# Kernel tuning notes

Hardware: AMD Instinct MI355X
Metric: run time of the kernel (lower is better)

Reference implementation:

```python
import math
import jax, jax.numpy as jnp
import numpy as np

B, T, C = 2, 2048, 1024
H, HKV, HD = 16, 4, 64  # n_head, n_kv_head, head_dim
G = H // HKV            # GQA groups
WS = 1024               # sliding window size
GATE_CH = 32


def setup_inputs() -> dict:
    key = jax.random.key(0)
    ks = jax.random.split(key, 8)
    x = jax.random.normal(ks[0], (B, T, C), dtype=jnp.float32)
    ve = jax.random.normal(ks[1], (B, T, HKV * HD), dtype=jnp.float32)
    # realistic RoPE tables: half head_dim frequencies
    d = HD // 2
    inv_freq = 1.0 / (10000.0 ** (jnp.arange(d, dtype=jnp.float32) / d))
    angles = jnp.arange(T, dtype=jnp.float32)[:, None] * inv_freq[None, :]  # (T, d)
    cos = jnp.cos(angles)[None, :, None, :]  # (1, T, 1, d)
    sin = jnp.sin(angles)[None, :, None, :]
    s = 0.02
    Wq = s * jax.random.normal(ks[2], (C, H * HD), dtype=jnp.float32)
    Wk = s * jax.random.normal(ks[3], (C, HKV * HD), dtype=jnp.float32)
    Wv = s * jax.random.normal(ks[4], (C, HKV * HD), dtype=jnp.float32)
    Wproj = s * jax.random.normal(ks[5], (C, C), dtype=jnp.float32)
    Wg = s * jax.random.normal(ks[6], (GATE_CH, HKV), dtype=jnp.float32)
    return {"x": x, "ve": ve, "cos": cos, "sin": sin,
            "Wq": Wq, "Wk": Wk, "Wv": Wv, "Wproj": Wproj, "Wg": Wg, "ws": WS}


def _rope(u, cos, sin):
    d = u.shape[-1] // 2
    u1, u2 = u[..., :d], u[..., d:]
    return jnp.concatenate([u1 * cos + u2 * sin, -u1 * sin + u2 * cos], axis=-1)


def _rmsnorm(u):
    eps = jnp.finfo(u.dtype).eps
    return u * jax.lax.rsqrt(jnp.mean(u * u, axis=-1, keepdims=True) + eps)


def reference(x, ve, cos, sin, Wq, Wk, Wv, Wproj, Wg, ws):
    b, t, c = x.shape
    q = (x @ Wq).reshape(b, t, H, HD)
    k = (x @ Wk).reshape(b, t, HKV, HD)
    v = (x @ Wv).reshape(b, t, HKV, HD)
    # value-embedding gate: 2*sigmoid over first 32 channels of x
    gate = 2.0 * jax.nn.sigmoid(x[..., :GATE_CH] @ Wg)  # (b, t, HKV)
    v = v + gate[..., None] * ve.reshape(b, t, HKV, HD)
    q = _rmsnorm(_rope(q, cos, sin))
    k = _rmsnorm(_rope(k, cos, sin))
    # GQA: view q as (b, t, HKV, G, HD), contract against shared k/v per kv-head
    qg = q.reshape(b, t, HKV, G, HD)
    scale = 1.0 / math.sqrt(HD)
    scores = jnp.einsum('bqhgd,bkhd->bhgqk', qg, k) * scale  # (b, HKV, G, t, t)
    pos = jnp.arange(t)
    # key j attends iff i - ws + 1 <= j <= i (sliding causal window)
    mask = (pos[None, :] >= pos[:, None] - ws + 1) & (pos[None, :] <= pos[:, None])
    scores = jnp.where(mask[None, None, None], scores, -jnp.inf)
    attn = jax.nn.softmax(scores, axis=-1)
    y = jnp.einsum('bhgqk,bkhd->bqhgd', attn, v).reshape(b, t, H * HD)
    return y @ Wproj
```

## Files before the change

kernel.cpp:

```cpp
#include <hip/hip_runtime.h>
#include <hip/hip_bf16.h>

#define Bq 2
#define Tq 2048
#define Cq 1024
#define Hq 16
#define HKVq 4
#define HDq 64
#define Gq 4
#define WSq 1024
#define GATE_CHq 32

typedef __attribute__((ext_vector_type(8))) short short8;
typedef __attribute__((ext_vector_type(4))) float f32x4;
typedef __attribute__((ext_vector_type(16))) float f32x16;
typedef __attribute__((ext_vector_type(2))) unsigned int u32x2;
typedef unsigned int u32;
typedef unsigned short u16;

#if __has_builtin(__builtin_amdgcn_exp2f)
#define EXP2(x) __builtin_amdgcn_exp2f(x)
#else
#define EXP2(x) exp2f(x)
#endif

__device__ __forceinline__ u16 f2bf(float f) {
  u32 u = __float_as_uint(f);
  u32 r = (u + 0x7FFFu + ((u >> 16) & 1u)) >> 16;
  return (u16)r;
}
__device__ __forceinline__ float bf2f(u16 u) {
  return __uint_as_float(((u32)u) << 16);
}

__device__ __forceinline__ void gl_lds16(const u16* g, u16* l) {
  __builtin_amdgcn_global_load_lds(
      (const u32 __attribute__((address_space(1)))*)g,
      (u32 __attribute__((address_space(3)))*)l, 16, 0, 0);
}

__global__ __launch_bounds__(256) void qkv_gemm_fused(
    const u16* __restrict__ A, const u16* __restrict__ Bt,
    const float* __restrict__ ve, const float* __restrict__ cosp,
    const float* __restrict__ sinp, const float* __restrict__ gatebuf,
    u16* __restrict__ Qb, u16* __restrict__ Kb, u16* __restrict__ Vtb) {
  __shared__ __attribute__((aligned(16))) u16 As[64 * 128];
  __shared__ __attribute__((aligned(16))) u16 Bs[128 * 128];

  const int bx = blockIdx.x;
  const int bm0 = blockIdx.y * 64, bn0 = bx * 128;
  const int tid = threadIdx.x;
  const int w = tid >> 6, lane = tid & 63;
  const int wm = (w >> 1) * 32, wn = (w & 1) * 64;
  const int quad = lane >> 4, l16 = lane & 15;
  const int K = 1024;

  f32x4 acc[2][4];
#pragma unroll
  for (int mt = 0; mt < 2; mt++)
#pragma unroll
    for (int nt = 0; nt < 4; nt++) acc[mt][nt] = (f32x4){0.f, 0.f, 0.f, 0.f};

  int goffA[4], goffB[8];
#pragma unroll
  for (int i = 0; i < 4; i++) {
    int s = i * 256 + tid;
    int m = s >> 4, gp = s & 15;
    goffA[i] = m * K + (gp ^ (m & 7)) * 8;
  }
#pragma unroll
  for (int i = 0; i < 8; i++) {
    int s = i * 256 + tid;
    int m = s >> 4, gp = s & 15;
    goffB[i] = m * K + (gp ^ (m & 7)) * 8;
  }
  const u16* Ab = A + (long)bm0 * K;
  const u16* Bb = Bt + (long)bn0 * K;

  for (int k0 = 0; k0 < K; k0 += 128) {
    __syncthreads();
#pragma unroll
    for (int i = 0; i < 4; i++)
      gl_lds16(Ab + goffA[i] + k0, &As[(i * 256 + w * 64) * 8]);
#pragma unroll
    for (int i = 0; i < 8; i++)
      gl_lds16(Bb + goffB[i] + k0, &Bs[(i * 256 + w * 64) * 8]);
    __syncthreads();

#pragma unroll
    for (int ks = 0; ks < 4; ks++) {
      short8 af[2], bf[4];
#pragma unroll
      for (int mt = 0; mt < 2; mt++) {
        int ml = wm + mt * 16 + l16;
        af[mt] = *(const short8*)&As[ml * 128 + (((ks * 4 + quad) ^ (ml & 7)) * 8)];
      }
#pragma unroll
      for (int nt = 0; nt < 4; nt++) {
        int nl = wn + nt * 16 + l16;
        bf[nt] = *(const short8*)&Bs[nl * 128 + (((ks * 4 + quad) ^ (nl & 7)) * 8)];
      }
#pragma unroll
      for (int mt = 0; mt < 2; mt++)
#pragma unroll
        for (int nt = 0; nt < 4; nt++)
          acc[mt][nt] = __builtin_amdgcn_mfma_f32_16x16x32_bf16(
              af[mt], bf[nt], acc[mt][nt], 0, 0, 0);
    }
  }

  const int b = bm0 >> 11;
  const int tseq0 = (bm0 & 2047) + wm;

  if (bx < 10) {
    u16* Dst;
    if (bx < 8) {
      int hh = bx * 2 + (w & 1);
      int hkv = hh >> 2, g = hh & 3;
      Dst = Qb + ((long)((b * 4 + hkv) * 4 + g) * Tq) * 64;
    } else {
      int kk = (bx - 8) * 2 + (w & 1);
      Dst = Kb + ((long)(b * 4 + kk) * Tq) * 64;
    }
#pragma unroll
    for (int mt = 0; mt < 2; mt++) {
#pragma unroll
      for (int r = 0; r < 4; r++) {
        int t = tseq0 + mt * 16 + quad * 4 + r;
        float c0 = cosp[t * 32 + l16];
        float s0 = sinp[t * 32 + l16];
        float c1 = cosp[t * 32 + 16 + l16];
        float s1 = sinp[t * 32 + 16 + l16];
        float a0 = acc[mt][0][r], a1 = acc[mt][1][r];
        float a2 = acc[mt][2][r], a3 = acc[mt][3][r];
        float rp0 = a0 * c0 + a2 * s0;
        float rp1 = a1 * c1 + a3 * s1;
        float rp2 = a2 * c0 - a0 * s0;
        float rp3 = a3 * c1 - a1 * s1;
        float ss = rp0 * rp0 + rp1 * rp1 + rp2 * rp2 + rp3 * rp3;
        ss += __shfl_xor(ss, 1);
        ss += __shfl_xor(ss, 2);
        ss += __shfl_xor(ss, 4);
        ss += __shfl_xor(ss, 8);
        float sc = rsqrtf(ss * (1.f / 64.f) + 1.1920928955078125e-07f);
        u16* drow = Dst + (long)t * 64;
        drow[l16] = f2bf(rp0 * sc);
        drow[16 + l16] = f2bf(rp1 * sc);
        drow[32 + l16] = f2bf(rp2 * sc);
        drow[48 + l16] = f2bf(rp3 * sc);
      }
    }
  } else {
    int kk = (bx - 10) * 2 + (w & 1);
    u16* Dst = Vtb + ((long)(b * 4 + kk) * 64) * Tq;
#pragma unroll
    for (int mt = 0; mt < 2; mt++) {
      float vals[4][4];
#pragma unroll
      for (int r = 0; r < 4; r++) {
        int t = tseq0 + mt * 16 + quad * 4 + r;
        long bt = (long)b * Tq + t;
        float gv = gatebuf[bt * 4 + kk];
        const float* verow = ve + bt * 256 + kk * 64;
#pragma unroll
        for (int nt = 0; nt < 4; nt++)
          vals[nt][r] = acc[mt][nt][r] + gv * verow[nt * 16 + l16];
      }
      int t0m = tseq0 + mt * 16 + quad * 4;
#pragma unroll
      for (int nt = 0; nt < 4; nt++) {
        int d = nt * 16 + l16;
        union { short4 v; u16 u[4]; } p;
#pragma unroll
        for (int r = 0; r < 4; r++) p.u[r] = f2bf(vals[nt][r]);
        *(short4*)(Dst + (long)d * Tq + t0m) = p.v;
      }
    }
  }
}

__global__ __launch_bounds__(256) void gemm_proj(
    const u16* __restrict__ A, const u16* __restrict__ Bt,
    float* __restrict__ C, int M, int N, int K) {
  __shared__ __attribute__((aligned(16))) u16 As[64 * 128];
  __shared__ __attribute__((aligned(16))) u16 Bs[128 * 128];

  const int bm0 = blockIdx.y * 64, bn0 = blockIdx.x * 128;
  const int tid = threadIdx.x;
  const int w = tid >> 6, lane = tid & 63;
  const int wm = (w >> 1) * 32, wn = (w & 1) * 64;
  const int quad = lane >> 4, l16 = lane & 15;

  f32x4 acc[2][4];
#pragma unroll
  for (int mt = 0; mt < 2; mt++)
#pragma unroll
    for (int nt = 0; nt < 4; nt++) acc[mt][nt] = (f32x4){0.f, 0.f, 0.f, 0.f};

  int goffA[4], goffB[8];
#pragma unroll
  for (int i = 0; i < 4; i++) {
    int s = i * 256 + tid;
    int m = s >> 4, gp = s & 15;
    goffA[i] = m * K + (gp ^ (m & 7)) * 8;
  }
#pragma unroll
  for (int i = 0; i < 8; i++) {
    int s = i * 256 + tid;
    int m = s >> 4, gp = s & 15;
    goffB[i] = m * K + (gp ^ (m & 7)) * 8;
  }
  const u16* Ab = A + (long)bm0 * K;
  const u16* Bb = Bt + (long)bn0 * K;

  for (int k0 = 0; k0 < K; k0 += 128) {
    __syncthreads();
#pragma unroll
    for (int i = 0; i < 4; i++)
      gl_lds16(Ab + goffA[i] + k0, &As[(i * 256 + w * 64) * 8]);
#pragma unroll
    for (int i = 0; i < 8; i++)
      gl_lds16(Bb + goffB[i] + k0, &Bs[(i * 256 + w * 64) * 8]);
    __syncthreads();

#pragma unroll
    for (int ks = 0; ks < 4; ks++) {
      short8 af[2], bf[4];
#pragma unroll
      for (int mt = 0; mt < 2; mt++) {
        int ml = wm + mt * 16 + l16;
        af[mt] = *(const short8*)&As[ml * 128 + (((ks * 4 + quad) ^ (ml & 7)) * 8)];
      }
#pragma unroll
      for (int nt = 0; nt < 4; nt++) {
        int nl = wn + nt * 16 + l16;
        bf[nt] = *(const short8*)&Bs[nl * 128 + (((ks * 4 + quad) ^ (nl & 7)) * 8)];
      }
#pragma unroll
      for (int mt = 0; mt < 2; mt++)
#pragma unroll
        for (int nt = 0; nt < 4; nt++)
          acc[mt][nt] = __builtin_amdgcn_mfma_f32_16x16x32_bf16(
              af[mt], bf[nt], acc[mt][nt], 0, 0, 0);
    }
  }

#pragma unroll
  for (int mt = 0; mt < 2; mt++)
#pragma unroll
    for (int nt = 0; nt < 4; nt++) {
      int row0 = bm0 + wm + mt * 16 + quad * 4;
      int col = bn0 + wn + nt * 16 + l16;
#pragma unroll
      for (int r = 0; r < 4; r++)
        C[(long)(row0 + r) * N + col] = acc[mt][nt][r];
    }
}

__global__ __launch_bounds__(256) void prep(
    const float* __restrict__ x, u16* __restrict__ xb,
    const float* __restrict__ Wq, const float* __restrict__ Wk,
    const float* __restrict__ Wv, const float* __restrict__ Wproj,
    const float* __restrict__ Wg, u16* __restrict__ Dqkv,
    u16* __restrict__ Dproj, float* __restrict__ gatebuf) {
  __shared__ float tile[64][65];
  int bx = blockIdx.x;
  int tid = threadIdx.x;
  if (bx < 2048) {
    int i = (bx * 256 + tid) * 8;
    float4 a = *(const float4*)(x + i);
    float4 b = *(const float4*)(x + i + 4);
    union { short8 v; u16 u[8]; } o;
    o.u[0] = f2bf(a.x); o.u[1] = f2bf(a.y); o.u[2] = f2bf(a.z); o.u[3] = f2bf(a.w);
    o.u[4] = f2bf(b.x); o.u[5] = f2bf(b.y); o.u[6] = f2bf(b.z); o.u[7] = f2bf(b.w);
    *(short8*)(xb + i) = o.v;
    return;
  }
  if (bx >= 2688) {
    int p = (bx - 2688) * 256 + tid;
    int bt = p >> 2, kk = p & 3;
    const float* xr = x + (long)bt * Cq;
    float dot = 0.f;
#pragma unroll
    for (int i = 0; i < GATE_CHq; i++) dot += xr[i] * Wg[i * HKVq + kk];
    gatebuf[p] = 2.f / (1.f + expf(-dot));
    return;
  }
  int wb = bx - 2048;
  int obx = wb >> 4;
  int k0 = (wb & 15) * 64;
  const float* S;
  u16* Dst;
  int N, nb;
  if (obx < 16)      { S = Wq;    N = 1024; nb = obx;      Dst = Dqkv; }
  else if (obx < 20) { S = Wk;    N = 256;  nb = obx - 16; Dst = Dqkv + 1024 * 1024; }
  else if (obx < 24) { S = Wv;    N = 256;  nb = obx - 20; Dst = Dqkv + 1280 * 1024; }
  else               { S = Wproj; N = 1024; nb = obx - 24; Dst = Dproj; }
  int n0 = nb * 64;
#pragma unroll
  for (int i = 0; i < 16; i++) {
    int idx = i * 256 + tid;
    int kl = idx >> 6, nl = idx & 63;
    tile[kl][nl] = S[(long)(k0 + kl) * N + n0 + nl];
  }
  __syncthreads();
#pragma unroll
  for (int i = 0; i < 16; i++) {
    int idx = i * 256 + tid;
    int nl = idx >> 6, kl = idx & 63;
    Dst[(long)(n0 + nl) * 1024 + k0 + kl] = f2bf(tile[kl][nl]);
  }
}

#define CEXP 0.18033688011112042f
#define CEXP8 1.4426950408889634f

template <bool MASK>
__device__ __forceinline__ void attn_tile32(
    int k0, int q0, int l31, int hl, const u16* __restrict__ Ks,
    const u16* __restrict__ Vts, const short8 (&QB)[4], f32x16& O0, f32x16& O1,
    float& lsum) {
  const int qpos = q0 + l31;
#pragma unroll
  for (int c = 0; c < 4; c++) {
    const int key = c * 32 + l31;
    f32x16 S;
#pragma unroll
    for (int i = 0; i < 16; i++) S[i] = 0.f;
    __builtin_amdgcn_s_setprio(1);
#pragma unroll
    for (int s = 0; s < 4; s++) {
      short8 kf = *(const short8*)&Ks[key * 64 + (((s * 2 + hl) ^ (key & 7)) * 8)];
      S = __builtin_amdgcn_mfma_f32_32x32x16_bf16(kf, QB[s], S, 0, 0, 0);
    }
    __builtin_amdgcn_s_setprio(0);
    const int kb = k0 + c * 32 + 4 * hl;
    float p[16];
    float la0 = 0.f, la1 = 0.f;
#pragma unroll
    for (int r = 0; r < 16; r++) {
      float sv = S[r];
      if (MASK) {
        int kpos = kb + (r & 3) + 8 * (r >> 2);
        u32 diff = (u32)(qpos - kpos);
        sv = (diff < (u32)WSq) ? sv : -1e30f;
      }
      float pv = EXP2(__builtin_fmaf(sv, CEXP, -CEXP8));
      if (r & 1) la1 += pv; else la0 += pv;
      p[r] = pv;
    }
    lsum += la0 + la1;
    u32 w[8];
#pragma unroll
    for (int i = 0; i < 8; i++) {
      u32 lo = __float_as_uint(p[2 * i]) + 0x8000u;
      u32 hi = __float_as_uint(p[2 * i + 1]) + 0x8000u;
      w[i] = __builtin_amdgcn_perm(hi, lo, 0x07060302u);
    }
    u32x2 r02 = __builtin_amdgcn_permlane32_swap(w[0], w[2], false, false);
    u32x2 r13 = __builtin_amdgcn_permlane32_swap(w[1], w[3], false, false);
    u32x2 r46 = __builtin_amdgcn_permlane32_swap(w[4], w[6], false, false);
    u32x2 r57 = __builtin_amdgcn_permlane32_swap(w[5], w[7], false, false);
    union { short8 s8; u32 u[4]; } f0, f1;
    f0.u[0] = r02[0]; f0.u[1] = r13[0]; f0.u[2] = r02[1]; f0.u[3] = r13[1];
    f1.u[0] = r46[0]; f1.u[1] = r57[0]; f1.u[2] = r46[1]; f1.u[3] = r57[1];
    const int d0 = l31, d1 = 32 + l31;
    const int sw = (l31 & 7);
    __builtin_amdgcn_s_setprio(1);
#pragma unroll
    for (int kc = 0; kc < 2; kc++) {
      int grp = c * 4 + kc * 2 + hl;
      short8 v0 = *(const short8*)&Vts[d0 * 128 + ((grp ^ sw) * 8)];
      short8 v1 = *(const short8*)&Vts[d1 * 128 + ((grp ^ sw) * 8)];
      const short8 pf = kc ? f1.s8 : f0.s8;
      O0 = __builtin_amdgcn_mfma_f32_32x32x16_bf16(v0, pf, O0, 0, 0, 0);
      O1 = __builtin_amdgcn_mfma_f32_32x32x16_bf16(v1, pf, O1, 0, 0, 0);
    }
    __builtin_amdgcn_s_setprio(0);
  }
}

__global__ __launch_bounds__(256, 2) void attn_mfma(
    const u16* __restrict__ Qb, const u16* __restrict__ Kb,
    const u16* __restrict__ Vtb, u16* __restrict__ Yb) {
  __shared__ __attribute__((aligned(16))) u16 Ks[2][128 * 64];
  __shared__ __attribute__((aligned(16))) u16 Vts[2][64 * 128];

  int bid = blockIdx.x;
  int bh = bid & 7;
  int qt32 = bid >> 3;
  int hkv = bh & 3;
  int b = bh >> 2;
  int q0 = qt32 * 32;
  int tid = threadIdx.x;
  int g = tid >> 6;
  int lane = tid & 63;
  int l31 = lane & 31;
  int hl = lane >> 5;

  short8 QB[4];
  {
    const u16* qb =
        Qb + ((long)((bh * 4 + g) * Tq + q0 + l31)) * 64 + hl * 8;
#pragma unroll
    for (int s = 0; s < 4; s++) QB[s] = *(const short8*)(qb + s * 16);
  }

  f32x16 O0, O1;
#pragma unroll
  for (int i = 0; i < 16; i++) { O0[i] = 0.f; O1[i] = 0.f; }
  float lsum = 0.f;

  int lo = q0 - (WSq - 1);
  int st = (lo < 0 ? 0 : lo) >> 7;
  int et = (q0 + 31) >> 7;

  const u16* Kbase = Kb + ((long)bh * Tq) * 64;
  const u16* Vbase = Vtb + ((long)bh * 64) * Tq;

  int rowoffK[4], rowoffV[4];
#pragma unroll
  for (int i = 0; i < 4; i++) {
    int s = i * 256 + tid;
    int kr = s >> 3, kgp = s & 7;
    rowoffK[i] = kr * 64 + (kgp ^ (kr & 7)) * 8;
    int d = s >> 4, vgp = s & 15;
    rowoffV[i] = d * Tq + (vgp ^ (d & 7)) * 8;
  }

  {
    int k0 = st << 7;
#pragma unroll
    for (int i = 0; i < 4; i++) {
      gl_lds16(Kbase + (long)k0 * 64 + rowoffK[i], &Ks[0][(i * 256 + g * 64) * 8]);
      gl_lds16(Vbase + k0 + rowoffV[i], &Vts[0][(i * 256 + g * 64) * 8]);
    }
  }
  __syncthreads();

  int cur = 0;
  for (int kt = st; kt <= et; kt++) {
    int k0 = kt << 7;
    if (kt < et) {
      int k0n = k0 + 128;
#pragma unroll
      for (int i = 0; i < 4; i++) {
        gl_lds16(Kbase + (long)k0n * 64 + rowoffK[i],
                 &Ks[cur ^ 1][(i * 256 + g * 64) * 8]);
        gl_lds16(Vbase + k0n + rowoffV[i],
                 &Vts[cur ^ 1][(i * 256 + g * 64) * 8]);
      }
    }
    bool needC = (k0 + 127 > q0);
    bool needW = (k0 < q0 - 992);
    if (needC || needW) {
      attn_tile32<true>(k0, q0, l31, hl, Ks[cur], Vts[cur], QB, O0, O1, lsum);
    } else {
      attn_tile32<false>(k0, q0, l31, hl, Ks[cur], Vts[cur], QB, O0, O1, lsum);
    }
    __syncthreads();
    cur ^= 1;
  }

  lsum += __shfl_xor(lsum, 32);
  float invl = 1.f / lsum;

  int h = hkv * 4 + g;
  u16* yrow = Yb + ((long)(b * Tq + q0 + l31)) * 1024 + h * 64;
#pragma unroll
  for (int g4 = 0; g4 < 4; g4++) {
    union { short4 v; u16 u[4]; } pk0, pk1;
#pragma unroll
    for (int i = 0; i < 4; i++) {
      pk0.u[i] = f2bf(O0[g4 * 4 + i] * invl);
      pk1.u[i] = f2bf(O1[g4 * 4 + i] * invl);
    }
    int dA = 8 * g4 + 4 * hl;
    *(short4*)(yrow + dA) = pk0.v;
    *(short4*)(yrow + 32 + dA) = pk1.v;
  }
}

extern "C" void kernel_launch(void* const* d_in, const int* in_sizes, int n_in,
                              void* d_out, int out_size, void* d_ws,
                              size_t ws_size, hipStream_t stream) {
  const float* x     = (const float*)d_in[0];
  const float* ve    = (const float*)d_in[1];
  const float* cosp  = (const float*)d_in[2];
  const float* sinp  = (const float*)d_in[3];
  const float* Wq    = (const float*)d_in[4];
  const float* Wk    = (const float*)d_in[5];
  const float* Wv    = (const float*)d_in[6];
  const float* Wproj = (const float*)d_in[7];
  const float* Wg    = (const float*)d_in[8];

  char* base = (char*)d_ws;
  u16* xb      = (u16*)(base);
  u16* Yb      = xb;
  u16* WqkvT   = (u16*)(base + 8388608);
  u16* WprojT  = (u16*)(base + 11534336);
  u16* Qb      = (u16*)(base + 13631488);
  u16* Kb      = (u16*)(base + 22020096);
  u16* Vtb     = (u16*)(base + 24117248);
  float* gateb = (float*)(base + 26214400);
  float* out = (float*)d_out;

  prep<<<2752, 256, 0, stream>>>(x, xb, Wq, Wk, Wv, Wproj, Wg, WqkvT, WprojT,
                                 gateb);
  qkv_gemm_fused<<<dim3(12, 64), 256, 0, stream>>>(xb, WqkvT, ve, cosp, sinp,
                                                   gateb, Qb, Kb, Vtb);
  attn_mfma<<<512, 256, 0, stream>>>(Qb, Kb, Vtb, Yb);
  gemm_proj<<<dim3(8, 64), 256, 0, stream>>>(Yb, WprojT, out, 4096, 1024, 1024);
}
```

Measured before the change: 163.5 us.

## Fuse all four stages into one cooperative persistent kernel with grid syncs

Replaces the four launches (prep, QKV GEMM, attention, projection) with a single cooperative kernel of 512 blocks that steps through the stages, separated by grid.sync and thread fences. The QKV GEMM stage is retiled to 128x128 blocks so that 384 blocks cover the work, and the other stages reuse the existing tiling on a shared LDS buffer. The aim is to remove launch gaps and per-kernel tails. In exchange the grid-wide barriers add cost, 128 blocks sit idle during the GEMM stage, and occupancy is capped by the 64KB shared buffer. If the cooperative launch fails, it falls back to the original four launches.

```diff
diff --git a/kernel.cpp b/kernel.cpp
--- a/kernel.cpp
+++ b/kernel.cpp
@@ -1,5 +1,8 @@
 #include <hip/hip_runtime.h>
 #include <hip/hip_bf16.h>
+#include <hip/hip_cooperative_groups.h>
+
+namespace cg = cooperative_groups;
 
 #define Bq 2
 #define Tq 2048
@@ -29,14 +32,451 @@
   u32 r = (u + 0x7FFFu + ((u >> 16) & 1u)) >> 16;
   return (u16)r;
 }
-__device__ __forceinline__ float bf2f(u16 u) {
-  return __uint_as_float(((u32)u) << 16);
-}
 
 __device__ __forceinline__ void gl_lds16(const u16* g, u16* l) {
   __builtin_amdgcn_global_load_lds(
       (const u32 __attribute__((address_space(1)))*)g,
       (u32 __attribute__((address_space(3)))*)l, 16, 0, 0);
+}
+
+#define CEXP 0.18033688011112042f
+#define CEXP8 1.4426950408889634f
+
+template <bool MASK>
+__device__ __forceinline__ void attn_tile32(
+    int k0, int q0, int l31, int hl, const u16* __restrict__ Ks,
+    const u16* __restrict__ Vts, const short8 (&QB)[4], f32x16& O0, f32x16& O1,
+    float& lsum) {
+  const int qpos = q0 + l31;
+#pragma unroll
+  for (int c = 0; c < 4; c++) {
+    const int key = c * 32 + l31;
+    f32x16 S;
+#pragma unroll
+    for (int i = 0; i < 16; i++) S[i] = 0.f;
+    __builtin_amdgcn_s_setprio(1);
+#pragma unroll
+    for (int s = 0; s < 4; s++) {
+      short8 kf = *(const short8*)&Ks[key * 64 + (((s * 2 + hl) ^ (key & 7)) * 8)];
+      S = __builtin_amdgcn_mfma_f32_32x32x16_bf16(kf, QB[s], S, 0, 0, 0);
+    }
+    __builtin_amdgcn_s_setprio(0);
+    const int kb = k0 + c * 32 + 4 * hl;
+    float p[16];
+    float la0 = 0.f, la1 = 0.f;
+#pragma unroll
+    for (int r = 0; r < 16; r++) {
+      float sv = S[r];
+      if (MASK) {
+        int kpos = kb + (r & 3) + 8 * (r >> 2);
+        u32 diff = (u32)(qpos - kpos);
+        sv = (diff < (u32)WSq) ? sv : -1e30f;
+      }
+      float pv = EXP2(__builtin_fmaf(sv, CEXP, -CEXP8));
+      if (r & 1) la1 += pv; else la0 += pv;
+      p[r] = pv;
+    }
+    lsum += la0 + la1;
+    u32 w8[8];
+#pragma unroll
+    for (int i = 0; i < 8; i++) {
+      u32 lo = __float_as_uint(p[2 * i]) + 0x8000u;
+      u32 hi = __float_as_uint(p[2 * i + 1]) + 0x8000u;
+      w8[i] = __builtin_amdgcn_perm(hi, lo, 0x07060302u);
+    }
+    u32x2 r02 = __builtin_amdgcn_permlane32_swap(w8[0], w8[2], false, false);
+    u32x2 r13 = __builtin_amdgcn_permlane32_swap(w8[1], w8[3], false, false);
+    u32x2 r46 = __builtin_amdgcn_permlane32_swap(w8[4], w8[6], false, false);
+    u32x2 r57 = __builtin_amdgcn_permlane32_swap(w8[5], w8[7], false, false);
+    union { short8 s8; u32 u[4]; } f0, f1;
+    f0.u[0] = r02[0]; f0.u[1] = r13[0]; f0.u[2] = r02[1]; f0.u[3] = r13[1];
+    f1.u[0] = r46[0]; f1.u[1] = r57[0]; f1.u[2] = r46[1]; f1.u[3] = r57[1];
+    const int d0 = l31, d1 = 32 + l31;
+    const int sw = (l31 & 7);
+    __builtin_amdgcn_s_setprio(1);
+#pragma unroll
+    for (int kc = 0; kc < 2; kc++) {
+      int grp = c * 4 + kc * 2 + hl;
+      short8 v0 = *(const short8*)&Vts[d0 * 128 + ((grp ^ sw) * 8)];
+      short8 v1 = *(const short8*)&Vts[d1 * 128 + ((grp ^ sw) * 8)];
+      const short8 pf = kc ? f1.s8 : f0.s8;
+      O0 = __builtin_amdgcn_mfma_f32_32x32x16_bf16(v0, pf, O0, 0, 0, 0);
+      O1 = __builtin_amdgcn_mfma_f32_32x32x16_bf16(v1, pf, O1, 0, 0, 0);
+    }
+    __builtin_amdgcn_s_setprio(0);
+  }
+}
+
+__global__ __launch_bounds__(256, 2) void mega(
+    const float* __restrict__ x, const float* __restrict__ ve,
+    const float* __restrict__ cosp, const float* __restrict__ sinp,
+    const float* __restrict__ Wq, const float* __restrict__ Wk,
+    const float* __restrict__ Wv, const float* __restrict__ Wproj,
+    const float* __restrict__ Wg, u16* __restrict__ xb,
+    u16* __restrict__ WqkvT, u16* __restrict__ WprojT, u16* __restrict__ Qb,
+    u16* __restrict__ Kb, u16* __restrict__ Vtb, float* __restrict__ gateb,
+    float* __restrict__ out) {
+  __shared__ __attribute__((aligned(16))) u16 smem[32768];
+  cg::grid_group grid = cg::this_grid();
+
+  const int bid = blockIdx.x;
+  const int tid = threadIdx.x;
+  const int w = tid >> 6, lane = tid & 63;
+  const int quad = lane >> 4, l16 = lane & 15;
+
+  for (int vb = bid; vb < 2752; vb += 512) {
+    if (vb < 2048) {
+      int i = (vb * 256 + tid) * 8;
+      float4 a = *(const float4*)(x + i);
+      float4 b4 = *(const float4*)(x + i + 4);
+      union { short8 v; u16 u[8]; } o;
+      o.u[0] = f2bf(a.x); o.u[1] = f2bf(a.y); o.u[2] = f2bf(a.z); o.u[3] = f2bf(a.w);
+      o.u[4] = f2bf(b4.x); o.u[5] = f2bf(b4.y); o.u[6] = f2bf(b4.z); o.u[7] = f2bf(b4.w);
+      *(short8*)(xb + i) = o.v;
+    } else if (vb >= 2688) {
+      int p = (vb - 2688) * 256 + tid;
+      int bt = p >> 2, kk = p & 3;
+      const float* xr = x + (long)bt * Cq;
+      float dot = 0.f;
+#pragma unroll
+      for (int i = 0; i < GATE_CHq; i++) dot += xr[i] * Wg[i * HKVq + kk];
+      gateb[p] = 2.f / (1.f + expf(-dot));
+    } else {
+      float* tile = (float*)smem;
+      int wb = vb - 2048;
+      int obx = wb >> 4;
+      int k0 = (wb & 15) * 64;
+      const float* S;
+      u16* Dst;
+      int N, nb;
+      if (obx < 16)      { S = Wq;    N = 1024; nb = obx;      Dst = WqkvT; }
+      else if (obx < 20) { S = Wk;    N = 256;  nb = obx - 16; Dst = WqkvT + 1024 * 1024; }
+      else if (obx < 24) { S = Wv;    N = 256;  nb = obx - 20; Dst = WqkvT + 1280 * 1024; }
+      else               { S = Wproj; N = 1024; nb = obx - 24; Dst = WprojT; }
+      int n0 = nb * 64;
+#pragma unroll
+      for (int i = 0; i < 16; i++) {
+        int idx = i * 256 + tid;
+        int kl = idx >> 6, nl = idx & 63;
+        tile[kl * 65 + nl] = S[(long)(k0 + kl) * N + n0 + nl];
+      }
+      __syncthreads();
+#pragma unroll
+      for (int i = 0; i < 16; i++) {
+        int idx = i * 256 + tid;
+        int nl = idx >> 6, kl = idx & 63;
+        Dst[(long)(n0 + nl) * 1024 + k0 + kl] = f2bf(tile[kl * 65 + nl]);
+      }
+      __syncthreads();
+    }
+  }
+  __threadfence();
+  grid.sync();
+  __threadfence();
+
+  if (bid < 384) {
+    const int bx = bid % 12;
+    const int bm0 = (bid / 12) * 128, bn0 = bx * 128;
+    const int wm = (w >> 1) * 64, wn = (w & 1) * 64;
+    const int K = 1024;
+    u16* sA = smem;
+    u16* sB = smem + 16384;
+
+    f32x4 acc[4][4];
+#pragma unroll
+    for (int mt = 0; mt < 4; mt++)
+#pragma unroll
+      for (int nt = 0; nt < 4; nt++) acc[mt][nt] = (f32x4){0.f, 0.f, 0.f, 0.f};
+
+    int goff[8];
+#pragma unroll
+    for (int i = 0; i < 8; i++) {
+      int s = i * 256 + tid;
+      int m = s >> 4, gp = s & 15;
+      goff[i] = m * K + (gp ^ (m & 7)) * 8;
+    }
+    const u16* Ab = xb + (long)bm0 * K;
+    const u16* Bb = WqkvT + (long)bn0 * K;
+
+    for (int k0 = 0; k0 < K; k0 += 128) {
+      __syncthreads();
+#pragma unroll
+      for (int i = 0; i < 8; i++)
+        gl_lds16(Ab + goff[i] + k0, &sA[(i * 256 + w * 64) * 8]);
+#pragma unroll
+      for (int i = 0; i < 8; i++)
+        gl_lds16(Bb + goff[i] + k0, &sB[(i * 256 + w * 64) * 8]);
+      __syncthreads();
+
+#pragma unroll
+      for (int ks = 0; ks < 4; ks++) {
+        short8 af[4], bf[4];
+#pragma unroll
+        for (int mt = 0; mt < 4; mt++) {
+          int ml = wm + mt * 16 + l16;
+          af[mt] = *(const short8*)&sA[ml * 128 + (((ks * 4 + quad) ^ (ml & 7)) * 8)];
+        }
+#pragma unroll
+        for (int nt = 0; nt < 4; nt++) {
+          int nl = wn + nt * 16 + l16;
+          bf[nt] = *(const short8*)&sB[nl * 128 + (((ks * 4 + quad) ^ (nl & 7)) * 8)];
+        }
+#pragma unroll
+        for (int mt = 0; mt < 4; mt++)
+#pragma unroll
+          for (int nt = 0; nt < 4; nt++)
+            acc[mt][nt] = __builtin_amdgcn_mfma_f32_16x16x32_bf16(
+                af[mt], bf[nt], acc[mt][nt], 0, 0, 0);
+      }
+    }
+
+    const int b = bm0 >> 11;
+    const int tseq0 = (bm0 & 2047) + wm;
+
+    if (bx < 10) {
+      u16* Dst;
+      if (bx < 8) {
+        int hh = bx * 2 + (w & 1);
+        int hkv = hh >> 2, g = hh & 3;
+        Dst = Qb + ((long)((b * 4 + hkv) * 4 + g) * Tq) * 64;
+      } else {
+        int kk = (bx - 8) * 2 + (w & 1);
+        Dst = Kb + ((long)(b * 4 + kk) * Tq) * 64;
+      }
+#pragma unroll
+      for (int mt = 0; mt < 4; mt++) {
+#pragma unroll
+        for (int r = 0; r < 4; r++) {
+          int t = tseq0 + mt * 16 + quad * 4 + r;
+          float c0 = cosp[t * 32 + l16];
+          float s0 = sinp[t * 32 + l16];
+          float c1 = cosp[t * 32 + 16 + l16];
+          float s1 = sinp[t * 32 + 16 + l16];
+          float a0 = acc[mt][0][r], a1 = acc[mt][1][r];
+          float a2 = acc[mt][2][r], a3 = acc[mt][3][r];
+          float rp0 = a0 * c0 + a2 * s0;
+          float rp1 = a1 * c1 + a3 * s1;
+          float rp2 = a2 * c0 - a0 * s0;
+          float rp3 = a3 * c1 - a1 * s1;
+          float ss = rp0 * rp0 + rp1 * rp1 + rp2 * rp2 + rp3 * rp3;
+          ss += __shfl_xor(ss, 1);
+          ss += __shfl_xor(ss, 2);
+          ss += __shfl_xor(ss, 4);
+          ss += __shfl_xor(ss, 8);
+          float sc = rsqrtf(ss * (1.f / 64.f) + 1.1920928955078125e-07f);
+          u16* drow = Dst + (long)t * 64;
+          drow[l16] = f2bf(rp0 * sc);
+          drow[16 + l16] = f2bf(rp1 * sc);
+          drow[32 + l16] = f2bf(rp2 * sc);
+          drow[48 + l16] = f2bf(rp3 * sc);
+        }
+      }
+    } else {
+      int kk = (bx - 10) * 2 + (w & 1);
+      u16* Dst = Vtb + ((long)(b * 4 + kk) * 64) * Tq;
+#pragma unroll
+      for (int mt = 0; mt < 4; mt++) {
+        float vals[4][4];
+#pragma unroll
+        for (int r = 0; r < 4; r++) {
+          int t = tseq0 + mt * 16 + quad * 4 + r;
+          long bt = (long)b * Tq + t;
+          float gv = gateb[bt * 4 + kk];
+          const float* verow = ve + bt * 256 + kk * 64;
+#pragma unroll
+          for (int nt = 0; nt < 4; nt++)
+            vals[nt][r] = acc[mt][nt][r] + gv * verow[nt * 16 + l16];
+        }
+        int t0m = tseq0 + mt * 16 + quad * 4;
+#pragma unroll
+        for (int nt = 0; nt < 4; nt++) {
+          int d = nt * 16 + l16;
+          union { short4 v; u16 u[4]; } pk;
+#pragma unroll
+          for (int r = 0; r < 4; r++) pk.u[r] = f2bf(vals[nt][r]);
+          *(short4*)(Dst + (long)d * Tq + t0m) = pk.v;
+        }
+      }
+    }
+  }
+  __threadfence();
+  grid.sync();
+  __threadfence();
+
+  {
+    u16* KsB = smem;
+    u16* VtB = smem + 16384;
+
+    int bh = bid & 7;
+    int qt32 = bid >> 3;
+    int hkv = bh & 3;
+    int b = bh >> 2;
+    int q0 = qt32 * 32;
+    int l31 = lane & 31;
+    int hl = lane >> 5;
+
+    short8 QB[4];
+    {
+      const u16* qb =
+          Qb + ((long)((bh * 4 + w) * Tq + q0 + l31)) * 64 + hl * 8;
+#pragma unroll
+      for (int s = 0; s < 4; s++) QB[s] = *(const short8*)(qb + s * 16);
+    }
+
+    f32x16 O0, O1;
+#pragma unroll
+    for (int i = 0; i < 16; i++) { O0[i] = 0.f; O1[i] = 0.f; }
+    float lsum = 0.f;
+
+    int lo = q0 - (WSq - 1);
+    int st = (lo < 0 ? 0 : lo) >> 7;
+    int et = (q0 + 31) >> 7;
+
+    const u16* Kbase = Kb + ((long)bh * Tq) * 64;
+    const u16* Vbase = Vtb + ((long)bh * 64) * Tq;
+
+    int rowoffK[4], rowoffV[4];
+#pragma unroll
+    for (int i = 0; i < 4; i++) {
+      int s = i * 256 + tid;
+      int kr = s >> 3, kgp = s & 7;
+      rowoffK[i] = kr * 64 + (kgp ^ (kr & 7)) * 8;
+      int d = s >> 4, vgp = s & 15;
+      rowoffV[i] = d * Tq + (vgp ^ (d & 7)) * 8;
+    }
+
+    {
+      int k0 = st << 7;
+#pragma unroll
+      for (int i = 0; i < 4; i++) {
+        gl_lds16(Kbase + (long)k0 * 64 + rowoffK[i],
+                 KsB + (i * 256 + w * 64) * 8);
+        gl_lds16(Vbase + k0 + rowoffV[i], VtB + (i * 256 + w * 64) * 8);
+      }
+    }
+    __syncthreads();
+
+    int cur = 0;
+    for (int kt = st; kt <= et; kt++) {
+      int k0 = kt << 7;
+      if (kt < et) {
+        int k0n = k0 + 128;
+        int nb = cur ^ 1;
+#pragma unroll
+        for (int i = 0; i < 4; i++) {
+          gl_lds16(Kbase + (long)k0n * 64 + rowoffK[i],
+                   KsB + nb * 8192 + (i * 256 + w * 64) * 8);
+          gl_lds16(Vbase + k0n + rowoffV[i],
+                   VtB + nb * 8192 + (i * 256 + w * 64) * 8);
+        }
+      }
+      bool needC = (k0 + 127 > q0);
+      bool needW = (k0 < q0 - 992);
+      if (needC || needW) {
+        attn_tile32<true>(k0, q0, l31, hl, KsB + cur * 8192, VtB + cur * 8192,
+                          QB, O0, O1, lsum);
+      } else {
+        attn_tile32<false>(k0, q0, l31, hl, KsB + cur * 8192, VtB + cur * 8192,
+                           QB, O0, O1, lsum);
+      }
+      __syncthreads();
+      cur ^= 1;
+    }
+
+    lsum += __shfl_xor(lsum, 32);
+    float invl = 1.f / lsum;
+
+    int h = hkv * 4 + w;
+    u16* yrow = xb + ((long)(b * Tq + q0 + l31)) * 1024 + h * 64;
+#pragma unroll
+    for (int g4 = 0; g4 < 4; g4++) {
+      union { short4 v; u16 u[4]; } pk0, pk1;
+#pragma unroll
+      for (int i = 0; i < 4; i++) {
+        pk0.u[i] = f2bf(O0[g4 * 4 + i] * invl);
+        pk1.u[i] = f2bf(O1[g4 * 4 + i] * invl);
+      }
+      int dA = 8 * g4 + 4 * hl;
+      *(short4*)(yrow + dA) = pk0.v;
+      *(short4*)(yrow + 32 + dA) = pk1.v;
+    }
+  }
+  __threadfence();
+  grid.sync();
+  __threadfence();
+
+  {
+    const int bm0 = (bid >> 3) * 64, bn0 = (bid & 7) * 128;
+    const int wm = (w >> 1) * 32, wn = (w & 1) * 64;
+    const int K = 1024, N = 1024;
+    u16* sA = smem;
+    u16* sB = smem + 8192;
+
+    f32x4 acc[2][4];
+#pragma unroll
+    for (int mt = 0; mt < 2; mt++)
+#pragma unroll
+      for (int nt = 0; nt < 4; nt++) acc[mt][nt] = (f32x4){0.f, 0.f, 0.f, 0.f};
+
+    int goffA[4], goffB[8];
+#pragma unroll
+    for (int i = 0; i < 4; i++) {
+      int s = i * 256 + tid;
+      int m = s >> 4, gp = s & 15;
+      goffA[i] = m * K + (gp ^ (m & 7)) * 8;
+    }
+#pragma unroll
+    for (int i = 0; i < 8; i++) {
+      int s = i * 256 + tid;
+      int m = s >> 4, gp = s & 15;
+      goffB[i] = m * K + (gp ^ (m & 7)) * 8;
+    }
+    const u16* Ab = xb + (long)bm0 * K;
+    const u16* Bb = WprojT + (long)bn0 * K;
+
+    for (int k0 = 0; k0 < K; k0 += 128) {
+      __syncthreads();
+#pragma unroll
+      for (int i = 0; i < 4; i++)
+        gl_lds16(Ab + goffA[i] + k0, &sA[(i * 256 + w * 64) * 8]);
+#pragma unroll
+      for (int i = 0; i < 8; i++)
+        gl_lds16(Bb + goffB[i] + k0, &sB[(i * 256 + w * 64) * 8]);
+      __syncthreads();
+
+#pragma unroll
+      for (int ks = 0; ks < 4; ks++) {
+        short8 af[2], bf[4];
+#pragma unroll
+        for (int mt = 0; mt < 2; mt++) {
+          int ml = wm + mt * 16 + l16;
+          af[mt] = *(const short8*)&sA[ml * 128 + (((ks * 4 + quad) ^ (ml & 7)) * 8)];
+        }
+#pragma unroll
+        for (int nt = 0; nt < 4; nt++) {
+          int nl = wn + nt * 16 + l16;
+          bf[nt] = *(const short8*)&sB[nl * 128 + (((ks * 4 + quad) ^ (nl & 7)) * 8)];
+        }
+#pragma unroll
+        for (int mt = 0; mt < 2; mt++)
+#pragma unroll
+          for (int nt = 0; nt < 4; nt++)
+            acc[mt][nt] = __builtin_amdgcn_mfma_f32_16x16x32_bf16(
+                af[mt], bf[nt], acc[mt][nt], 0, 0, 0);
+      }
+    }
+
+#pragma unroll
+    for (int mt = 0; mt < 2; mt++)
+#pragma unroll
+      for (int nt = 0; nt < 4; nt++) {
+        int row0 = bm0 + wm + mt * 16 + quad * 4;
+        int col = bn0 + wn + nt * 16 + l16;
+#pragma unroll
+        for (int r = 0; r < 4; r++)
+          out[(long)(row0 + r) * N + col] = acc[mt][nt][r];
+      }
+  }
 }
 
 __global__ __launch_bounds__(256) void qkv_gemm_fused(
@@ -312,74 +752,6 @@
   }
 }
 
-#define CEXP 0.18033688011112042f
-#define CEXP8 1.4426950408889634f
-
-template <bool MASK>
-__device__ __forceinline__ void attn_tile32(
-    int k0, int q0, int l31, int hl, const u16* __restrict__ Ks,
-    const u16* __restrict__ Vts, const short8 (&QB)[4], f32x16& O0, f32x16& O1,
-    float& lsum) {
-  const int qpos = q0 + l31;
-#pragma unroll
-  for (int c = 0; c < 4; c++) {
-    const int key = c * 32 + l31;
-    f32x16 S;
-#pragma unroll
-    for (int i = 0; i < 16; i++) S[i] = 0.f;
-    __builtin_amdgcn_s_setprio(1);
-#pragma unroll
-    for (int s = 0; s < 4; s++) {
-      short8 kf = *(const short8*)&Ks[key * 64 + (((s * 2 + hl) ^ (key & 7)) * 8)];
-      S = __builtin_amdgcn_mfma_f32_32x32x16_bf16(kf, QB[s], S, 0, 0, 0);
-    }
-    __builtin_amdgcn_s_setprio(0);
-    const int kb = k0 + c * 32 + 4 * hl;
-    float p[16];
-    float la0 = 0.f, la1 = 0.f;
-#pragma unroll
-    for (int r = 0; r < 16; r++) {
-      float sv = S[r];
-      if (MASK) {
-        int kpos = kb + (r & 3) + 8 * (r >> 2);
-        u32 diff = (u32)(qpos - kpos);
-        sv = (diff < (u32)WSq) ? sv : -1e30f;
-      }
-      float pv = EXP2(__builtin_fmaf(sv, CEXP, -CEXP8));
-      if (r & 1) la1 += pv; else la0 += pv;
-      p[r] = pv;
-    }
-    lsum += la0 + la1;
-    u32 w[8];
-#pragma unroll
-    for (int i = 0; i < 8; i++) {
-      u32 lo = __float_as_uint(p[2 * i]) + 0x8000u;
-      u32 hi = __float_as_uint(p[2 * i + 1]) + 0x8000u;
-      w[i] = __builtin_amdgcn_perm(hi, lo, 0x07060302u);
-    }
-    u32x2 r02 = __builtin_amdgcn_permlane32_swap(w[0], w[2], false, false);
-    u32x2 r13 = __builtin_amdgcn_permlane32_swap(w[1], w[3], false, false);
-    u32x2 r46 = __builtin_amdgcn_permlane32_swap(w[4], w[6], false, false);
-    u32x2 r57 = __builtin_amdgcn_permlane32_swap(w[5], w[7], false, false);
-    union { short8 s8; u32 u[4]; } f0, f1;
-    f0.u[0] = r02[0]; f0.u[1] = r13[0]; f0.u[2] = r02[1]; f0.u[3] = r13[1];
-    f1.u[0] = r46[0]; f1.u[1] = r57[0]; f1.u[2] = r46[1]; f1.u[3] = r57[1];
-    const int d0 = l31, d1 = 32 + l31;
-    const int sw = (l31 & 7);
-    __builtin_amdgcn_s_setprio(1);
-#pragma unroll
-    for (int kc = 0; kc < 2; kc++) {
-      int grp = c * 4 + kc * 2 + hl;
-      short8 v0 = *(const short8*)&Vts[d0 * 128 + ((grp ^ sw) * 8)];
-      short8 v1 = *(const short8*)&Vts[d1 * 128 + ((grp ^ sw) * 8)];
-      const short8 pf = kc ? f1.s8 : f0.s8;
-      O0 = __builtin_amdgcn_mfma_f32_32x32x16_bf16(v0, pf, O0, 0, 0, 0);
-      O1 = __builtin_amdgcn_mfma_f32_32x32x16_bf16(v1, pf, O1, 0, 0, 0);
-    }
-    __builtin_amdgcn_s_setprio(0);
-  }
-}
-
 __global__ __launch_bounds__(256, 2) void attn_mfma(
     const u16* __restrict__ Qb, const u16* __restrict__ Kb,
     const u16* __restrict__ Vtb, u16* __restrict__ Yb) {
@@ -496,19 +868,28 @@
 
   char* base = (char*)d_ws;
   u16* xb      = (u16*)(base);
-  u16* Yb      = xb;
   u16* WqkvT   = (u16*)(base + 8388608);
   u16* WprojT  = (u16*)(base + 11534336);
   u16* Qb      = (u16*)(base + 13631488);
   u16* Kb      = (u16*)(base + 22020096);
   u16* Vtb     = (u16*)(base + 24117248);
   float* gateb = (float*)(base + 26214400);
-  float* out = (float*)d_out;
-
-  prep<<<2752, 256, 0, stream>>>(x, xb, Wq, Wk, Wv, Wproj, Wg, WqkvT, WprojT,
-                                 gateb);
-  qkv_gemm_fused<<<dim3(12, 64), 256, 0, stream>>>(xb, WqkvT, ve, cosp, sinp,
-                                                   gateb, Qb, Kb, Vtb);
-  attn_mfma<<<512, 256, 0, stream>>>(Qb, Kb, Vtb, Yb);
-  gemm_proj<<<dim3(8, 64), 256, 0, stream>>>(Yb, WprojT, out, 4096, 1024, 1024);
+  float* out   = (float*)d_out;
+
+  void* args[] = {(void*)&x,     (void*)&ve,    (void*)&cosp, (void*)&sinp,
+                  (void*)&Wq,    (void*)&Wk,    (void*)&Wv,   (void*)&Wproj,
+                  (void*)&Wg,    (void*)&xb,    (void*)&WqkvT,
+                  (void*)&WprojT,(void*)&Qb,    (void*)&Kb,   (void*)&Vtb,
+                  (void*)&gateb, (void*)&out};
+  hipError_t err = hipLaunchCooperativeKernel((const void*)mega, dim3(512),
+                                              dim3(256), args, 0, stream);
+  if (err != hipSuccess) {
+    prep<<<2752, 256, 0, stream>>>(x, xb, Wq, Wk, Wv, Wproj, Wg, WqkvT, WprojT,
+                                   gateb);
+    qkv_gemm_fused<<<dim3(12, 64), 256, 0, stream>>>(xb, WqkvT, ve, cosp, sinp,
+                                                     gateb, Qb, Kb, Vtb);
+    attn_mfma<<<512, 256, 0, stream>>>(Qb, Kb, Vtb, xb);
+    gemm_proj<<<dim3(8, 64), 256, 0, stream>>>(xb, WprojT, out, 4096, 1024,
+                                               1024);
+  }
 }
```

Result: slower. 612.7 us (+274.7%).
